# Optimization experiments

Hardware: AMD Instinct MI355X
Metric: run time of the kernel (lower is better)

The kernel has to match this reference:

```python
import jax, jax.numpy as jnp
import numpy as np

IN_DIM = 1024
OUT_DIM = 1024
NUM_EXPERTS = 8
TOP_K = 2


def setup_inputs() -> dict:
    key = jax.random.key(0)
    ks = jax.random.split(key, 5)
    s = 1.0 / np.sqrt(IN_DIM)
    x = jax.random.normal(ks[0], (4, 2048, IN_DIM), dtype=jnp.float32)
    Wg = jax.random.uniform(ks[1], (IN_DIM, NUM_EXPERTS), jnp.float32, -s, s)
    bg = jnp.zeros((NUM_EXPERTS,), jnp.float32)
    We = jax.random.uniform(ks[2], (NUM_EXPERTS, OUT_DIM, IN_DIM), jnp.float32, -s, s)
    be = jax.random.uniform(ks[3], (NUM_EXPERTS, OUT_DIM), jnp.float32, -s, s)
    return {"x": x, "Wg": Wg, "bg": bg, "We": We, "be": be}


def reference(x, Wg, bg, We, be):
    # gate: softmax over experts
    gate = jax.nn.softmax(x @ Wg + bg, axis=-1)            # [b, s, E]
    # top-k sparsification + renormalization (scatter via one-hot)
    topk_vals, topk_idx = jax.lax.top_k(gate, TOP_K)       # [b, s, K]
    onehot = jax.nn.one_hot(topk_idx, NUM_EXPERTS, dtype=gate.dtype)  # [b,s,K,E]
    gate_sparse = jnp.einsum("bsk,bske->bse", topk_vals, onehot)
    gate_sparse = gate_sparse / jnp.sum(gate_sparse, axis=-1, keepdims=True)
    # dense all-expert compute, then gate-weighted sum (faithful to source)
    y = jnp.einsum("bsi,eoi->bseo", x, We) + be[None, None, :, :].transpose(0, 1, 2, 3)  # [b,s,E,o]
    out = jnp.einsum("bseo,bse->bso", y, gate_sparse)
    return out
```

## Files before the change

### kernel.cpp

```cpp
#include <hip/hip_runtime.h>
#include <hip/hip_bf16.h>

#define TOKENS 8192
#define KDIM 1024
#define NDIM 1024
#define NEXP 8

typedef __attribute__((ext_vector_type(8))) short short8v;
typedef __attribute__((ext_vector_type(8))) unsigned short ushort8v;
typedef __attribute__((ext_vector_type(4))) float f32x4;

__device__ inline unsigned short f2bf(float f) {
  unsigned int u = __float_as_uint(f);
  u += 0x7fffu + ((u >> 16) & 1u);
  return (unsigned short)(u >> 16);
}

__device__ inline void gload_lds16(const void* g, void* l) {
  __builtin_amdgcn_global_load_lds(
      (const __attribute__((address_space(1))) unsigned int*)g,
      (__attribute__((address_space(3))) unsigned int*)l, 16, 0, 0);
}


__global__ __launch_bounds__(256) void gate_conv_kernel(
    const float* __restrict__ x, const float* __restrict__ Wg,
    const float* __restrict__ bg, const float* __restrict__ We,
    unsigned short* __restrict__ xb, unsigned short* __restrict__ Web,
    int* __restrict__ epacked, float2* __restrict__ wpair,
    int* __restrict__ hist, float* __restrict__ out) {
  int b = blockIdx.x;
  int tid = threadIdx.x;
  if (b >= 4352) {
    float4* o = reinterpret_cast<float4*>(out) + (size_t)(b - 4352) * 2048 + tid;
    float4 z = make_float4(0.f, 0.f, 0.f, 0.f);
#pragma unroll
    for (int i = 0; i < 8; ++i) o[i * 256] = z;
    return;
  }
  if (b >= 256) {
    size_t i = (size_t)(b - 256) * 256 + tid;
    const float4* s = reinterpret_cast<const float4*>(We + i * 8);
    float4 a = s[0], c = s[1];
    ushort8v v;
    v[0] = f2bf(a.x); v[1] = f2bf(a.y); v[2] = f2bf(a.z); v[3] = f2bf(a.w);
    v[4] = f2bf(c.x); v[5] = f2bf(c.y); v[6] = f2bf(c.z); v[7] = f2bf(c.w);
    *reinterpret_cast<ushort8v*>(Web + i * 8) = v;
    return;
  }
  __shared__ int lhist[16];
  if (tid < 16) lhist[tid] = 0;
  __syncthreads();
  int w = tid >> 6, lane = tid & 63;
  int tok0 = b * 32 + w * 8;

  for (int t = 0; t < 8; ++t) {
    int tok = tok0 + t;
    const float* xr = x + (size_t)tok * KDIM + lane * 16;
    float acc[NEXP] = {};
    ushort8v xv0, xv1;
#pragma unroll
    for (int j4 = 0; j4 < 4; ++j4) {
      float4 xv = *reinterpret_cast<const float4*>(xr + j4 * 4);
      float xs[4] = {xv.x, xv.y, xv.z, xv.w};
#pragma unroll
      for (int jj = 0; jj < 4; ++jj) {
        int k = lane * 16 + j4 * 4 + jj;
        const float4* wr = reinterpret_cast<const float4*>(Wg + k * NEXP);
        float4 w0 = wr[0], w1 = wr[1];
        float xf = xs[jj];
        acc[0] += xf * w0.x; acc[1] += xf * w0.y;
        acc[2] += xf * w0.z; acc[3] += xf * w0.w;
        acc[4] += xf * w1.x; acc[5] += xf * w1.y;
        acc[6] += xf * w1.z; acc[7] += xf * w1.w;
        int li = j4 * 4 + jj;
        unsigned short bv = f2bf(xf);
        if (li < 8) xv0[li] = bv; else xv1[li - 8] = bv;
      }
    }
    unsigned short* xrow = xb + (size_t)tok * KDIM + lane * 16;
    *reinterpret_cast<ushort8v*>(xrow) = xv0;
    *reinterpret_cast<ushort8v*>(xrow + 8) = xv1;
#pragma unroll
    for (int e = 0; e < NEXP; ++e) {
      acc[e] += __shfl_xor(acc[e], 1, 64);
      acc[e] += __shfl_xor(acc[e], 2, 64);
      acc[e] += __shfl_xor(acc[e], 4, 64);
      acc[e] += __shfl_xor(acc[e], 8, 64);
      acc[e] += __shfl_xor(acc[e], 16, 64);
      acc[e] += __shfl_xor(acc[e], 32, 64);
    }
    if (lane == 0) {
      float lg[NEXP];
#pragma unroll
      for (int e = 0; e < NEXP; ++e) lg[e] = acc[e] + bg[e];
      int e0 = 0;
#pragma unroll
      for (int e = 1; e < NEXP; ++e) if (lg[e] > lg[e0]) e0 = e;
      int e1 = -1;
#pragma unroll
      for (int e = 0; e < NEXP; ++e) {
        if (e == e0) continue;
        if (e1 < 0 || lg[e] > lg[e1]) e1 = e;
      }
      float tv = expf(lg[e1] - lg[e0]);
      float w0 = 1.0f / (1.0f + tv);
      float w1 = tv * w0;
      epacked[tok] = e0 | (e1 << 8);
      wpair[tok] = make_float2(w0, w1);
      atomicAdd(&lhist[e0], 1);
      atomicAdd(&lhist[8 + e1], 1);
    }
  }
  __syncthreads();
  if (tid < 16) hist[b * 16 + tid] = lhist[tid];
}

__global__ __launch_bounds__(256) void scatter_kernel(
    const int* __restrict__ hist, const int* __restrict__ epacked,
    const float2* __restrict__ wpair, int* __restrict__ counts,
    int* __restrict__ lists, float* __restrict__ wlists) {
  __shared__ int partial[16][17];
  __shared__ int base[16];
  __shared__ int cnt2[16];
  int tid = threadIdx.x;
  int b = blockIdx.x;
  int bin = tid & 15, grp = tid >> 4;
  int s = 0;
  for (int i = 0; i < 16; ++i) {
    int bb = grp * 16 + i;
    if (bb < b) s += hist[bb * 16 + bin];
  }
  partial[grp][bin] = s;
  if (tid < 16) cnt2[tid] = 0;
  __syncthreads();
  if (tid < 16) {
    int s2 = 0;
#pragma unroll
    for (int g = 0; g < 16; ++g) s2 += partial[g][tid];
    base[tid] = s2;
  }
  __syncthreads();
  if (tid < 64) {
    int tok = b * 32 + (tid >> 1);
    int slot = tid & 1;
    int ep = epacked[tok];
    int e = slot ? ((ep >> 8) & 255) : (ep & 255);
    float2 wp = wpair[tok];
    float wv = slot ? wp.y : wp.x;
    int bn = slot * 8 + e;
    int pos = base[bn] + atomicAdd(&cnt2[bn], 1);
    lists[bn * TOKENS + pos] = tok;
    wlists[bn * TOKENS + pos] = wv;
  }
  if (b == 255) {
    __syncthreads();
    if (tid < 16) counts[tid] = base[tid] + cnt2[tid];
  }
}

template <int PLAIN>
__global__ __launch_bounds__(512) void moe_gemm_wide(
    const unsigned short* __restrict__ xb, const unsigned short* __restrict__ Web,
    const float* __restrict__ be, const int* __restrict__ counts,
    const int* __restrict__ lists, const float* __restrict__ wlists,
    float* __restrict__ out, float* __restrict__ p1) {
  int bz = blockIdx.z;
  int e = bz & 7;
  int slot = bz >> 3;
  int cnt = counts[bz];
  int mbase = blockIdx.y * 128;
  if (mbase >= cnt) return;
  int nbase = blockIdx.x * 256;
  const int* lst = lists + bz * TOKENS;
  const float* wl = wlists + bz * TOKENS;

  __shared__ alignas(128) unsigned short lA[128 * 64];
  __shared__ alignas(128) unsigned short lB[256 * 64];

  int tid = threadIdx.x;
  int lane = tid & 63;
  int w = tid >> 6;
  int wm = w >> 2, wn = w & 3;
  int lm = lane & 15, lk = lane >> 4;

  const unsigned short* aga[2];
#pragma unroll
  for (int j = 0; j < 2; ++j) {
    int L = j * 512 + tid;
    int r = L >> 3, cs = L & 7;
    int c = cs ^ (r & 7);
    int gr = mbase + r; if (gr >= cnt) gr = cnt - 1;
    aga[j] = xb + (size_t)lst[gr] * KDIM + c * 8;
  }
  const unsigned short* bga[4];
#pragma unroll
  for (int j = 0; j < 4; ++j) {
    int L = j * 512 + tid;
    int r = L >> 3, cs = L & 7;
    int c = cs ^ (r & 7);
    bga[j] = Web + (size_t)e * (NDIM * KDIM) + (size_t)(nbase + r) * KDIM + c * 8;
  }

#define STAGE(kt)                                                             \
  {                                                                           \
    _Pragma("unroll") for (int j = 0; j < 2; ++j)                             \
      gload_lds16(aga[j] + (kt) * 64, (char*)lA + j * 8192 + w * 1024);       \
    _Pragma("unroll") for (int j = 0; j < 4; ++j)                             \
      gload_lds16(bga[j] + (kt) * 64, (char*)lB + j * 8192 + w * 1024);       \
  }

  f32x4 acc[4][4] = {};

#define COMPUTE                                                               \
  {                                                                           \
    _Pragma("unroll") for (int ks = 0; ks < 2; ++ks) {                        \
      short8v af[4], bfv[4];                                                  \
      _Pragma("unroll") for (int mi = 0; mi < 4; ++mi) {                      \
        int row = wm * 64 + mi * 16 + lm;                                     \
        int cs = (ks * 4 + lk) ^ (row & 7);                                   \
        af[mi] = *reinterpret_cast<const short8v*>(&lA[row * 64 + cs * 8]);   \
      }                                                                       \
      _Pragma("unroll") for (int nj = 0; nj < 4; ++nj) {                      \
        int row = wn * 64 + nj * 16 + lm;                                     \
        int cs = (ks * 4 + lk) ^ (row & 7);                                   \
        bfv[nj] = *reinterpret_cast<const short8v*>(&lB[row * 64 + cs * 8]);  \
      }                                                                       \
      _Pragma("unroll") for (int mi = 0; mi < 4; ++mi)                        \
        _Pragma("unroll") for (int nj = 0; nj < 4; ++nj)                      \
          acc[mi][nj] = __builtin_amdgcn_mfma_f32_16x16x32_bf16(              \
              af[mi], bfv[nj], acc[mi][nj], 0, 0, 0);                         \
    }                                                                         \
  }

  for (int kt = 0; kt < 16; ++kt) {
    __syncthreads();
    STAGE(kt);
    __syncthreads();
    COMPUTE;
  }
#undef STAGE
#undef COMPUTE

  float* dst = (PLAIN && slot) ? p1 : out;
  float bev[4];
#pragma unroll
  for (int nj = 0; nj < 4; ++nj)
    bev[nj] = be[e * NDIM + nbase + wn * 64 + nj * 16 + lm];
#pragma unroll
  for (int mi = 0; mi < 4; ++mi) {
#pragma unroll
    for (int r = 0; r < 4; ++r) {
      int grow = mbase + wm * 64 + mi * 16 + lk * 4 + r;
      if (grow >= cnt) continue;
      int tokn = lst[grow];
      float wgt = wl[grow];
      float* orow = dst + (size_t)tokn * NDIM + nbase + wn * 64 + lm;
#pragma unroll
      for (int nj = 0; nj < 4; ++nj) {
        float val = wgt * (acc[mi][nj][r] + bev[nj]);
        if (PLAIN) orow[nj * 16] = val;
        else       unsafeAtomicAdd(&orow[nj * 16], val);
      }
    }
  }
}

__global__ __launch_bounds__(256) void combine_kernel(
    float* __restrict__ out, const float* __restrict__ p1) {
  size_t i = (size_t)blockIdx.x * 256 + threadIdx.x;
  float4 a = reinterpret_cast<const float4*>(p1)[i];
  float4 b = reinterpret_cast<float4*>(out)[i];
  b.x += a.x; b.y += a.y; b.z += a.z; b.w += a.w;
  reinterpret_cast<float4*>(out)[i] = b;
}


__global__ __launch_bounds__(256) void gate_kernel(
    const float* __restrict__ x, const float* __restrict__ Wg,
    const float* __restrict__ bg, int* __restrict__ counts,
    int* __restrict__ lists, float* __restrict__ wlists) {
  int gtid = blockIdx.x * blockDim.x + threadIdx.x;
  int tok = gtid >> 6;
  int lane = threadIdx.x & 63;
  if (tok >= TOKENS) return;
  const float* xr = x + (size_t)tok * KDIM + lane * 16;
  float acc[NEXP] = {};
#pragma unroll
  for (int j4 = 0; j4 < 4; ++j4) {
    float4 xv = *reinterpret_cast<const float4*>(xr + j4 * 4);
    float xs[4] = {xv.x, xv.y, xv.z, xv.w};
#pragma unroll
    for (int jj = 0; jj < 4; ++jj) {
      int k = lane * 16 + j4 * 4 + jj;
      const float4* wr = reinterpret_cast<const float4*>(Wg + k * NEXP);
      float4 w0 = wr[0], w1 = wr[1];
      float xv1 = xs[jj];
      acc[0] += xv1 * w0.x; acc[1] += xv1 * w0.y;
      acc[2] += xv1 * w0.z; acc[3] += xv1 * w0.w;
      acc[4] += xv1 * w1.x; acc[5] += xv1 * w1.y;
      acc[6] += xv1 * w1.z; acc[7] += xv1 * w1.w;
    }
  }
#pragma unroll
  for (int e = 0; e < NEXP; ++e) {
    acc[e] += __shfl_xor(acc[e], 1, 64);
    acc[e] += __shfl_xor(acc[e], 2, 64);
    acc[e] += __shfl_xor(acc[e], 4, 64);
    acc[e] += __shfl_xor(acc[e], 8, 64);
    acc[e] += __shfl_xor(acc[e], 16, 64);
    acc[e] += __shfl_xor(acc[e], 32, 64);
  }
  if (lane == 0) {
    float lg[NEXP];
#pragma unroll
    for (int e = 0; e < NEXP; ++e) lg[e] = acc[e] + bg[e];
    int e0 = 0;
#pragma unroll
    for (int e = 1; e < NEXP; ++e) if (lg[e] > lg[e0]) e0 = e;
    int e1 = -1;
#pragma unroll
    for (int e = 0; e < NEXP; ++e) {
      if (e == e0) continue;
      if (e1 < 0 || lg[e] > lg[e1]) e1 = e;
    }
    float t = expf(lg[e1] - lg[e0]);
    float w0 = 1.0f / (1.0f + t);
    float w1 = t * w0;
    int p0 = atomicAdd(&counts[e0], 1);
    lists[e0 * TOKENS + p0] = tok;
    wlists[e0 * TOKENS + p0] = w0;
    int p1 = atomicAdd(&counts[NEXP + e1], 1);
    lists[(NEXP + e1) * TOKENS + p1] = tok;
    wlists[(NEXP + e1) * TOKENS + p1] = w1;
  }
}

template <int ACCUM>
__global__ __launch_bounds__(256) void moe_gemm(
    const float* __restrict__ x, const float* __restrict__ We,
    const float* __restrict__ be, const int* __restrict__ counts,
    const int* __restrict__ lists, const float* __restrict__ wlists,
    float* __restrict__ out, int slot) {
  int e = blockIdx.z;
  int cnt = counts[slot * NEXP + e];
  int mbase = blockIdx.y * 128;
  if (mbase >= cnt) return;
  int nbase = blockIdx.x * 128;
  const int* lst = lists + (slot * NEXP + e) * TOKENS;
  const float* wl = wlists + (slot * NEXP + e) * TOKENS;
  __shared__ ushort8v lA[1024];
  __shared__ ushort8v lB[1024];
  int tid = threadIdx.x;
  int lane = tid & 63;
  int w = tid >> 6;
  int wm = w >> 1, wn = w & 1;
  const float* aptr[4];
  const float* bptr[4];
  int sw[4];
#pragma unroll
  for (int i = 0; i < 4; ++i) {
    int c = i * 256 + tid;
    int r = c >> 3, cc = c & 7;
    int gr = mbase + r;
    if (gr >= cnt) gr = cnt - 1;
    int tokn = lst[gr];
    aptr[i] = x + (size_t)tokn * KDIM + cc * 8;
    bptr[i] = We + (size_t)e * (NDIM * KDIM) + (size_t)(nbase + r) * KDIM + cc * 8;
    sw[i] = r * 8 + (cc ^ (r & 7));
  }
  f32x4 acc[4][4] = {};
  int lm = lane & 15, lk = lane >> 4;
  for (int kt = 0; kt < KDIM / 64; ++kt) {
    __syncthreads();
#pragma unroll
    for (int i = 0; i < 4; ++i) {
      float4 f0 = *reinterpret_cast<const float4*>(aptr[i] + kt * 64);
      float4 f1 = *reinterpret_cast<const float4*>(aptr[i] + kt * 64 + 4);
      ushort8v v;
      v[0] = f2bf(f0.x); v[1] = f2bf(f0.y); v[2] = f2bf(f0.z); v[3] = f2bf(f0.w);
      v[4] = f2bf(f1.x); v[5] = f2bf(f1.y); v[6] = f2bf(f1.z); v[7] = f2bf(f1.w);
      lA[sw[i]] = v;
      float4 g0 = *reinterpret_cast<const float4*>(bptr[i] + kt * 64);
      float4 g1 = *reinterpret_cast<const float4*>(bptr[i] + kt * 64 + 4);
      ushort8v u;
      u[0] = f2bf(g0.x); u[1] = f2bf(g0.y); u[2] = f2bf(g0.z); u[3] = f2bf(g0.w);
      u[4] = f2bf(g1.x); u[5] = f2bf(g1.y); u[6] = f2bf(g1.z); u[7] = f2bf(g1.w);
      lB[sw[i]] = u;
    }
    __syncthreads();
#pragma unroll
    for (int ks = 0; ks < 2; ++ks) {
      short8v af[4], bfv[4];
#pragma unroll
      for (int mi = 0; mi < 4; ++mi) {
        int row = wm * 64 + mi * 16 + lm;
        int cidx = (ks * 4 + lk) ^ (row & 7);
        af[mi] = *reinterpret_cast<const short8v*>(&lA[row * 8 + cidx]);
      }
#pragma unroll
      for (int nj = 0; nj < 4; ++nj) {
        int row = wn * 64 + nj * 16 + lm;
        int cidx = (ks * 4 + lk) ^ (row & 7);
        bfv[nj] = *reinterpret_cast<const short8v*>(&lB[row * 8 + cidx]);
      }
#pragma unroll
      for (int mi = 0; mi < 4; ++mi)
#pragma unroll
        for (int nj = 0; nj < 4; ++nj)
          acc[mi][nj] = __builtin_amdgcn_mfma_f32_16x16x32_bf16(
              af[mi], bfv[nj], acc[mi][nj], 0, 0, 0);
    }
  }
  float bev[4];
#pragma unroll
  for (int nj = 0; nj < 4; ++nj)
    bev[nj] = be[e * NDIM + nbase + wn * 64 + nj * 16 + lm];
#pragma unroll
  for (int mi = 0; mi < 4; ++mi) {
#pragma unroll
    for (int r = 0; r < 4; ++r) {
      int grow = mbase + wm * 64 + mi * 16 + lk * 4 + r;
      if (grow >= cnt) continue;
      int tokn = lst[grow];
      float wgt = wl[grow];
      float* orow = out + (size_t)tokn * NDIM + nbase + wn * 64 + lm;
#pragma unroll
      for (int nj = 0; nj < 4; ++nj) {
        float val = wgt * (acc[mi][nj][r] + bev[nj]);
        if (ACCUM) orow[nj * 16] += val;
        else       orow[nj * 16] = val;
      }
    }
  }
}


extern "C" void kernel_launch(void* const* d_in, const int* in_sizes, int n_in,
                              void* d_out, int out_size, void* d_ws, size_t ws_size,
                              hipStream_t stream) {
  const float* x  = (const float*)d_in[0];
  const float* Wg = (const float*)d_in[1];
  const float* bg = (const float*)d_in[2];
  const float* We = (const float*)d_in[3];
  const float* be = (const float*)d_in[4];
  float* out = (float*)d_out;

  char* p = (char*)d_ws;
  int*   counts = (int*)p;                 p += 256;
  int*   lists  = (int*)p;                 p += (size_t)16 * TOKENS * 4;
  float* wlists = (float*)p;               p += (size_t)16 * TOKENS * 4;
  int*   epacked = (int*)p;                p += (size_t)TOKENS * 4;
  float2* wpair  = (float2*)p;             p += (size_t)TOKENS * 8;
  int*   hist    = (int*)p;                p += 256 * 16 * 4;
  unsigned short* xbuf = (unsigned short*)p; p += (size_t)TOKENS * KDIM * 2;
  unsigned short* Webf = (unsigned short*)p; p += (size_t)NEXP * NDIM * KDIM * 2;
  size_t need_mid = (size_t)(p - (char*)d_ws);
  float* part1 = (float*)p;                p += (size_t)TOKENS * NDIM * 4;
  size_t need_fast = (size_t)(p - (char*)d_ws);

  dim3 ggrid(NDIM / 256, 16, 16);
  if (ws_size >= need_fast) {
    gate_conv_kernel<<<4352, 256, 0, stream>>>(
        x, Wg, bg, We, xbuf, Webf, epacked, wpair, hist, out);
    scatter_kernel<<<256, 256, 0, stream>>>(hist, epacked, wpair, counts, lists, wlists);
    moe_gemm_wide<1><<<ggrid, 512, 0, stream>>>(
        xbuf, Webf, be, counts, lists, wlists, out, part1);
    combine_kernel<<<TOKENS * NDIM / 4 / 256, 256, 0, stream>>>(out, part1);
  } else if (ws_size >= need_mid) {
    gate_conv_kernel<<<5376, 256, 0, stream>>>(
        x, Wg, bg, We, xbuf, Webf, epacked, wpair, hist, out);
    scatter_kernel<<<256, 256, 0, stream>>>(hist, epacked, wpair, counts, lists, wlists);
    moe_gemm_wide<0><<<ggrid, 512, 0, stream>>>(
        xbuf, Webf, be, counts, lists, wlists, out, out);
  } else {
    dim3 grid(NDIM / 128, TOKENS / 128, NEXP);
    hipMemsetAsync(d_ws, 0, 64, stream);
    gate_kernel<<<TOKENS / 4, 256, 0, stream>>>(x, Wg, bg, counts, lists, wlists);
    moe_gemm<0><<<grid, 256, 0, stream>>>(x, We, be, counts, lists, wlists, out, 0);
    moe_gemm<1><<<grid, 256, 0, stream>>>(x, We, be, counts, lists, wlists, out, 1);
  }
}
```

Before: 118.1 us.

## Double-buffer LDS with BK=32 tiles and async prefetch in MoE GEMM

Cuts the K tile from 64 to 32 and splits LDS into two buffers, so global-to-LDS loads for tile k+2 are in flight while tile k is computed. The per-iteration double __syncthreads becomes explicit vmcnt waits plus raw s_barrier, and the XOR swizzle is reworked for the 32-wide rows. MFMA blocks are wrapped in setprio and sched_barrier. This doubles the number of barrier rounds and depends on the manual waitcnt values being correct for the number of outstanding loads.

```diff
diff --git a/kernel.cpp b/kernel.cpp
--- a/kernel.cpp
+++ b/kernel.cpp
@@ -175,8 +175,8 @@
   const int* lst = lists + bz * TOKENS;
   const float* wl = wlists + bz * TOKENS;
 
-  __shared__ alignas(128) unsigned short lA[128 * 64];
-  __shared__ alignas(128) unsigned short lB[256 * 64];
+  __shared__ alignas(128) unsigned short lA[2][128 * 32];
+  __shared__ alignas(128) unsigned short lB[2][256 * 32];
 
   int tid = threadIdx.x;
   int lane = tid & 63;
@@ -184,61 +184,66 @@
   int wm = w >> 2, wn = w & 3;
   int lm = lane & 15, lk = lane >> 4;
 
-  const unsigned short* aga[2];
+  const unsigned short* aga;
+  {
+    int r = tid >> 2, cs = tid & 3;
+    int c = cs ^ ((r >> 1) & 3);
+    int gr = mbase + r; if (gr >= cnt) gr = cnt - 1;
+    aga = xb + (size_t)lst[gr] * KDIM + c * 8;
+  }
+  const unsigned short* bga[2];
 #pragma unroll
   for (int j = 0; j < 2; ++j) {
     int L = j * 512 + tid;
-    int r = L >> 3, cs = L & 7;
-    int c = cs ^ (r & 7);
-    int gr = mbase + r; if (gr >= cnt) gr = cnt - 1;
-    aga[j] = xb + (size_t)lst[gr] * KDIM + c * 8;
-  }
-  const unsigned short* bga[4];
-#pragma unroll
-  for (int j = 0; j < 4; ++j) {
-    int L = j * 512 + tid;
-    int r = L >> 3, cs = L & 7;
-    int c = cs ^ (r & 7);
+    int r = L >> 2, cs = L & 3;
+    int c = cs ^ ((r >> 1) & 3);
     bga[j] = Web + (size_t)e * (NDIM * KDIM) + (size_t)(nbase + r) * KDIM + c * 8;
   }
 
-#define STAGE(kt)                                                             \
+#define STAGE(buf, kt)                                                        \
   {                                                                           \
+    gload_lds16(aga + (kt) * 32, (char*)lA[buf] + w * 1024);                  \
     _Pragma("unroll") for (int j = 0; j < 2; ++j)                             \
-      gload_lds16(aga[j] + (kt) * 64, (char*)lA + j * 8192 + w * 1024);       \
-    _Pragma("unroll") for (int j = 0; j < 4; ++j)                             \
-      gload_lds16(bga[j] + (kt) * 64, (char*)lB + j * 8192 + w * 1024);       \
+      gload_lds16(bga[j] + (kt) * 32, (char*)lB[buf] + j * 8192 + w * 1024);  \
   }
 
   f32x4 acc[4][4] = {};
 
-#define COMPUTE                                                               \
+#define COMPUTE(buf)                                                          \
   {                                                                           \
-    _Pragma("unroll") for (int ks = 0; ks < 2; ++ks) {                        \
-      short8v af[4], bfv[4];                                                  \
-      _Pragma("unroll") for (int mi = 0; mi < 4; ++mi) {                      \
-        int row = wm * 64 + mi * 16 + lm;                                     \
-        int cs = (ks * 4 + lk) ^ (row & 7);                                   \
-        af[mi] = *reinterpret_cast<const short8v*>(&lA[row * 64 + cs * 8]);   \
-      }                                                                       \
-      _Pragma("unroll") for (int nj = 0; nj < 4; ++nj) {                      \
-        int row = wn * 64 + nj * 16 + lm;                                     \
-        int cs = (ks * 4 + lk) ^ (row & 7);                                   \
-        bfv[nj] = *reinterpret_cast<const short8v*>(&lB[row * 64 + cs * 8]);  \
-      }                                                                       \
-      _Pragma("unroll") for (int mi = 0; mi < 4; ++mi)                        \
-        _Pragma("unroll") for (int nj = 0; nj < 4; ++nj)                      \
-          acc[mi][nj] = __builtin_amdgcn_mfma_f32_16x16x32_bf16(              \
-              af[mi], bfv[nj], acc[mi][nj], 0, 0, 0);                         \
+    short8v af[4], bfv[4];                                                    \
+    _Pragma("unroll") for (int mi = 0; mi < 4; ++mi) {                        \
+      int row = wm * 64 + mi * 16 + lm;                                       \
+      int cs = lk ^ ((row >> 1) & 3);                                         \
+      af[mi] = *reinterpret_cast<const short8v*>(&lA[buf][row * 32 + cs * 8]); \
     }                                                                         \
-  }
-
-  for (int kt = 0; kt < 16; ++kt) {
-    __syncthreads();
-    STAGE(kt);
-    __syncthreads();
-    COMPUTE;
-  }
+    _Pragma("unroll") for (int nj = 0; nj < 4; ++nj) {                        \
+      int row = wn * 64 + nj * 16 + lm;                                       \
+      int cs = lk ^ ((row >> 1) & 3);                                         \
+      bfv[nj] = *reinterpret_cast<const short8v*>(&lB[buf][row * 32 + cs * 8]); \
+    }                                                                         \
+    asm volatile("s_waitcnt lgkmcnt(0)" ::: "memory");                        \
+    __builtin_amdgcn_sched_barrier(0);                                        \
+    __builtin_amdgcn_s_setprio(1);                                            \
+    _Pragma("unroll") for (int mi = 0; mi < 4; ++mi)                          \
+      _Pragma("unroll") for (int nj = 0; nj < 4; ++nj)                        \
+        acc[mi][nj] = __builtin_amdgcn_mfma_f32_16x16x32_bf16(                \
+            af[mi], bfv[nj], acc[mi][nj], 0, 0, 0);                           \
+    __builtin_amdgcn_s_setprio(0);                                            \
+  }
+
+  STAGE(0, 0);
+  STAGE(1, 1);
+  for (int kt = 0; kt < 31; ++kt) {
+    asm volatile("s_waitcnt vmcnt(3)" ::: "memory");
+    asm volatile("s_barrier" ::: "memory");
+    if ((kt & 1) == 0) COMPUTE(0) else COMPUTE(1);
+    asm volatile("s_barrier" ::: "memory");
+    if (kt < 30) STAGE(kt & 1, kt + 2);
+  }
+  asm volatile("s_waitcnt vmcnt(0)" ::: "memory");
+  asm volatile("s_barrier" ::: "memory");
+  COMPUTE(1);
 #undef STAGE
 #undef COMPUTE
 
```

Result: slower. 142.2 us (+20.5%).
